# Kernel tuning notes

Hardware: AMD Instinct MI355X
Metric: run time of the kernel (lower is better)

## Reference

```python
import jax, jax.numpy as jnp
import numpy as np

H = 8          # num_heads
BM = 128       # block_size_m
BN = 128       # block_size_n
EPS = 1e-6
CAUSAL = True  # config.causal


def setup_inputs() -> dict:
    key = jax.random.key(0)
    ks = jax.random.split(key, 5)
    B, N, D = 1, 2048, 512
    s = 1.0 / np.sqrt(D)
    # small-scale x so projected points mostly stay inside the Poincare ball
    x = jax.random.normal(ks[0], (B, N, D), jnp.float32) * 0.05
    return {
        'x': x,
        'c': jnp.ones((1,), jnp.float32),
        'Wq': jax.random.normal(ks[1], (D, D), jnp.float32) * s,
        'bq': jnp.zeros((D,), jnp.float32),
        'Wk': jax.random.normal(ks[2], (D, D), jnp.float32) * s,
        'bk': jnp.zeros((D,), jnp.float32),
        'Wv': jax.random.normal(ks[3], (D, D), jnp.float32) * s,
        'bv': jnp.zeros((D,), jnp.float32),
        'Wo': jax.random.normal(ks[4], (D, D), jnp.float32) * s,
        'bo': jnp.zeros((D,), jnp.float32),
    }


def reference(x, c, Wq, bq, Wk, bk, Wv, bv, Wo, bo):
    B, N, D = x.shape
    Dh = D // H
    cc = jnp.clip(jnp.abs(c), 1e-6)            # (1,) learned curvature, abs+clamp as in torch
    sqrt_c = jnp.sqrt(jnp.clip(cc, EPS))

    def proj(W, b):
        return (x @ W + b).reshape(B, N, H, Dh).transpose(0, 2, 1, 3)  # (B,H,N,Dh)

    q, k, v = proj(Wq, bq), proj(Wk, bk), proj(Wv, bv)

    # Poincare distance: ||q-k||^2 expanded via norms (same math as explicit diff tensor)
    qn = (q ** 2).sum(-1)                      # (B,H,N)
    kn = (k ** 2).sum(-1)                      # (B,H,N)
    qk = jnp.einsum('bhmd,bhnd->bhmn', q, k)   # (B,H,N,N)
    diff_sq = jnp.clip(qn[..., :, None] + kn[..., None, :] - 2.0 * qk, 0.0)
    denom = jnp.clip((1.0 - cc * qn)[..., :, None] * (1.0 - cc * kn)[..., None, :], EPS)
    arg = jnp.clip(1.0 + 2.0 * cc * diff_sq / denom, 1.0 + EPS)
    scores = -jnp.arccosh(arg) / sqrt_c        # (B,H,N,N)

    # block-wise softmax: each 128x128 block subtracts ITS OWN max (faithful to torch code,
    # which omits cross-block max rescaling), then exp-sums are accumulated across blocks.
    nbm, nbn = N // BM, N // BN
    s = scores.reshape(B, H, nbm, BM, nbn, BN)
    row = jnp.arange(nbm)[:, None]
    col = jnp.arange(nbn)[None, :]
    skip = (col > row) if CAUSAL else jnp.zeros((nbm, nbn), bool)   # skipped upper blocks
    diag = (col == row) if CAUSAL else jnp.zeros((nbm, nbn), bool)
    tri = jnp.triu(jnp.ones((BM, BN), bool), 1)
    mask = skip[:, None, :, None] | (diag[:, None, :, None] & tri[None, :, None, :])  # (nbm,BM,nbn,BN)

    s_masked = jnp.where(mask, -jnp.inf, s)
    bmax = s_masked.max(axis=-1, keepdims=True)                      # per-block-row max over BN
    bmax = jnp.where(jnp.isfinite(bmax), bmax, 0.0)                  # skipped blocks -> safe
    e = jnp.where(mask, 0.0, jnp.exp(s - bmax))                      # (B,H,nbm,BM,nbn,BN)

    normalizer = jnp.clip(e.sum(axis=(4, 5)).reshape(B, H, N), EPS)  # (B,H,N)
    vb = v.reshape(B, H, nbn, BN, Dh)
    out = jnp.einsum('bhrmcn,bhcnd->bhrmd', e, vb).reshape(B, H, N, Dh)
    out = out / normalizer[..., None]
    out = out.transpose(0, 2, 1, 3).reshape(B, N, D)
    return out @ Wo + bo
```

## Files before the change

### kernel.cpp

```cpp
#include <hip/hip_runtime.h>
#include <math.h>

#define D_MODEL 512
#define NHEADS  8
#define NSEQ    2048
#define NBLK    16
#define NCHUNK  72
#define EPSF    1e-6f
#define WPLANE  262144

typedef _Float16 v8h __attribute__((ext_vector_type(8)));
typedef _Float16 v4h __attribute__((ext_vector_type(4)));
typedef float    v4f __attribute__((ext_vector_type(4)));

static __device__ __forceinline__ v4f mfma16h(v8h a, v8h b, v4f c) {
  return __builtin_amdgcn_mfma_f32_16x16x32_f16(a, b, c, 0, 0, 0);
}

__global__ __launch_bounds__(256) void prep_w(const float* __restrict__ W0,
                                              const float* __restrict__ W1,
                                              const float* __restrict__ W2,
                                              const float* __restrict__ W3,
                                              _Float16* __restrict__ Wth) {
  __shared__ float T[64][68];
  const int z = blockIdx.z;
  const float* W = (z == 0) ? W0 : (z == 1) ? W1 : (z == 2) ? W2 : W3;
  const int kb = blockIdx.x * 64;
  const int nb = blockIdx.y * 64;
  const int tid = threadIdx.x;
#pragma unroll
  for (int l = 0; l < 4; ++l) {
    int f = tid + l * 256;
    int row = f >> 4, c4 = f & 15;
    float4 v = *reinterpret_cast<const float4*>(&W[(size_t)(kb + row) * D_MODEL + nb + c4 * 4]);
    T[c4 * 4 + 0][row] = v.x; T[c4 * 4 + 1][row] = v.y;
    T[c4 * 4 + 2][row] = v.z; T[c4 * 4 + 3][row] = v.w;
  }
  __syncthreads();
  _Float16* oh = Wth + (size_t)z * WPLANE;
#pragma unroll
  for (int l = 0; l < 4; ++l) {
    int f = tid + l * 256;
    int n_ = f >> 4, k4 = f & 15;
    v4h h4;
    h4[0] = (_Float16)T[n_][k4 * 4 + 0];
    h4[1] = (_Float16)T[n_][k4 * 4 + 1];
    h4[2] = (_Float16)T[n_][k4 * 4 + 2];
    h4[3] = (_Float16)T[n_][k4 * 4 + 3];
    *reinterpret_cast<v4h*>(&oh[(size_t)(nb + n_) * D_MODEL + kb + k4 * 4]) = h4;
  }
}

__global__ __launch_bounds__(256) void qkv_gemm(
    const float* __restrict__ x, const _Float16* __restrict__ Wth,
    const float* __restrict__ bq, const float* __restrict__ bk,
    const float* __restrict__ bv,
    _Float16* __restrict__ Qp, _Float16* __restrict__ Kp,
    _Float16* __restrict__ Vp,
    float* __restrict__ Qn_, float* __restrict__ Kn_) {
  __shared__ _Float16 Ah[128][40], Bh[128][40];
  const int z = blockIdx.z;
  const _Float16* Bt = Wth + (size_t)z * WPLANE;
  const float* bias = (z == 0) ? bq : (z == 1) ? bk : bv;
  _Float16* outp = (z == 0) ? Qp : (z == 1) ? Kp : Vp;

  const int bx = blockIdx.x, by = blockIdx.y;
  const int tid = threadIdx.x;
  const int wid = tid >> 6, lane = tid & 63;
  const int wr = wid >> 1, wc = wid & 1;
  const int g = lane >> 4, lx = lane & 15;

  v4f acc[4][4];
#pragma unroll
  for (int i = 0; i < 4; ++i)
#pragma unroll
    for (int j = 0; j < 4; ++j) acc[i][j] = v4f{0.f, 0.f, 0.f, 0.f};

  for (int k0 = 0; k0 < 16; ++k0) {
    __syncthreads();
#pragma unroll
    for (int l = 0; l < 4; ++l) {
      int f = tid + l * 256;
      int row = f >> 3, c4 = f & 7;
      float4 a = *reinterpret_cast<const float4*>(&x[(size_t)(by * 128 + row) * D_MODEL + k0 * 32 + c4 * 4]);
      Ah[row][c4 * 4 + 0] = (_Float16)a.x;
      Ah[row][c4 * 4 + 1] = (_Float16)a.y;
      Ah[row][c4 * 4 + 2] = (_Float16)a.z;
      Ah[row][c4 * 4 + 3] = (_Float16)a.w;
    }
#pragma unroll
    for (int l = 0; l < 2; ++l) {
      int f = tid + l * 256;
      int row = f >> 2, c8 = f & 3;
      *reinterpret_cast<uint4*>(&Bh[row][c8 * 8]) =
          *reinterpret_cast<const uint4*>(&Bt[(size_t)(bx * 128 + row) * D_MODEL + k0 * 32 + c8 * 8]);
    }
    __syncthreads();
    v8h ah[4], bh[4];
#pragma unroll
    for (int i = 0; i < 4; ++i) {
      ah[i] = *reinterpret_cast<const v8h*>(&Ah[wr * 64 + i * 16 + lx][g * 8]);
      bh[i] = *reinterpret_cast<const v8h*>(&Bh[wc * 64 + i * 16 + lx][g * 8]);
    }
#pragma unroll
    for (int i = 0; i < 4; ++i)
#pragma unroll
      for (int j = 0; j < 4; ++j)
        acc[i][j] = mfma16h(ah[i], bh[j], acc[i][j]);
  }

  float np[4][4];
#pragma unroll
  for (int i = 0; i < 4; ++i)
#pragma unroll
    for (int r = 0; r < 4; ++r) np[i][r] = 0.f;

#pragma unroll
  for (int j = 0; j < 4; ++j) {
    const int col = bx * 128 + wc * 64 + j * 16 + lx;
    const float bj = bias[col];
#pragma unroll
    for (int i = 0; i < 4; ++i)
#pragma unroll
      for (int r = 0; r < 4; ++r) {
        const int row = by * 128 + wr * 64 + i * 16 + g * 4 + r;
        float v = acc[i][j][r] + bj;
        _Float16 hv = (_Float16)v;
        outp[(size_t)row * D_MODEL + col] = hv;
        float vr = (float)hv;
        np[i][r] = fmaf(vr, vr, np[i][r]);
      }
  }
  if (z < 2) {
    float* Nout = (z == 0) ? Qn_ : Kn_;
    const int hh = bx * 2 + wc;
#pragma unroll
    for (int i = 0; i < 4; ++i)
#pragma unroll
      for (int r = 0; r < 4; ++r) {
        float s = np[i][r];
        s += __shfl_xor(s, 1, 64);
        s += __shfl_xor(s, 2, 64);
        s += __shfl_xor(s, 4, 64);
        s += __shfl_xor(s, 8, 64);
        if (lx == 0)
          Nout[hh * NSEQ + by * 128 + wr * 64 + i * 16 + g * 4 + r] = s;
      }
  }
}

__global__ __launch_bounds__(256) void vt_prep(const ushort* __restrict__ Vb,
                                               ushort* __restrict__ Vtb) {
  __shared__ ushort T[64][72];
  const int nb = blockIdx.x * 64;
  const int h  = blockIdx.y;
  const int tid = threadIdx.x;
#pragma unroll
  for (int l = 0; l < 2; ++l) {
    int f = tid + l * 256;
    int row = f >> 3, c8 = f & 7;
    uint4 w = *reinterpret_cast<const uint4*>(&Vb[(size_t)(nb + row) * D_MODEL + h * 64 + c8 * 8]);
    const ushort* p = reinterpret_cast<const ushort*>(&w);
#pragma unroll
    for (int j = 0; j < 8; ++j) T[c8 * 8 + j][row] = p[j];
  }
  __syncthreads();
#pragma unroll
  for (int l = 0; l < 2; ++l) {
    int f = tid + l * 256;
    int d = f >> 3, n8 = f & 7;
    *reinterpret_cast<uint4*>(&Vtb[(size_t)(h * 64 + d) * NSEQ + nb + n8 * 8]) =
        *reinterpret_cast<const uint4*>(&T[d][n8 * 8]);
  }
}

__global__ __launch_bounds__(512, 4) void attn(
    const _Float16* __restrict__ Qp, const _Float16* __restrict__ Kp,
    const _Float16* __restrict__ Vtb, const float* __restrict__ Qn,
    const float* __restrict__ Kn, const float* __restrict__ cptr,
    float* __restrict__ Opart, float* __restrict__ Npart)
{
  __shared__ _Float16 Khs[128][68];
  __shared__ _Float16 Vs[64][136];
  __shared__ _Float16 Es[128][136];
  __shared__ float kns[128];

  const int bid = blockIdx.x;
  const int h    = bid & 7;
  const int pid2 = bid >> 3;
  int m = 0, base = 0;
  while (base + (m / 2 + 1) <= pid2) { base += m / 2 + 1; ++m; }
  const int c  = pid2 - base;
  const int n0 = 2 * c;
  const int n1 = (n0 + 1 < m) ? n0 + 1 : m;

  const int tid  = threadIdx.x;
  const int w    = tid >> 6;
  const int lane = tid & 63;
  const int g = lane >> 4, lx = lane & 15;

  const float cc = fmaxf(fabsf(cptr[0]), 1e-6f);
  const float is = rsqrtf(cc);
  const bool is_one = (cc == 1.0f);
  const float two_cc = 2.f * cc;

  const int krow = tid >> 3, kc8 = tid & 7;
  const int vrow = tid >> 4, vc8 = tid & 15;

  const _Float16* Kgh = Kp + h * 64;
  const _Float16* Vgh = Vtb + (size_t)(h * 64) * NSEQ;

  uint4 kpre0, kpre1, vpre0, vpre1;
  float knp = 0.f;
  {
    const _Float16* Kg = Kgh + (size_t)(n0 * 128) * D_MODEL;
    kpre0 = *reinterpret_cast<const uint4*>(&Kg[(size_t)krow * D_MODEL + kc8 * 8]);
    kpre1 = *reinterpret_cast<const uint4*>(&Kg[(size_t)(krow + 64) * D_MODEL + kc8 * 8]);
    vpre0 = *reinterpret_cast<const uint4*>(&Vgh[(size_t)vrow * NSEQ + n0 * 128 + vc8 * 8]);
    vpre1 = *reinterpret_cast<const uint4*>(&Vgh[(size_t)(vrow + 32) * NSEQ + n0 * 128 + vc8 * 8]);
    if (tid < 128) knp = Kn[h * NSEQ + n0 * 128 + tid];
  }
  *reinterpret_cast<uint4*>(&Khs[krow][kc8 * 8]) = kpre0;
  *reinterpret_cast<uint4*>(&Khs[krow + 64][kc8 * 8]) = kpre1;
  *reinterpret_cast<uint4*>(&Vs[vrow][vc8 * 8]) = vpre0;
  *reinterpret_cast<uint4*>(&Vs[vrow + 32][vc8 * 8]) = vpre1;
  if (tid < 128) kns[tid] = knp;
  __syncthreads();

  v8h aQ[2];
  {
    const size_t qoff = (size_t)(m * 128 + 16 * w + lx) * D_MODEL + h * 64 + g * 8;
    aQ[0] = *reinterpret_cast<const v8h*>(&Qp[qoff]);
    aQ[1] = *reinterpret_cast<const v8h*>(&Qp[qoff + 32]);
  }
  float qnr[4], qar[4];
#pragma unroll
  for (int r = 0; r < 4; ++r) {
    qnr[r] = Qn[h * NSEQ + m * 128 + 16 * w + g * 4 + r];
    qar[r] = fmaf(-cc, qnr[r], 1.f);
  }

  v4f o_acc[4];
#pragma unroll
  for (int td = 0; td < 4; ++td) o_acc[td] = v4f{0.f, 0.f, 0.f, 0.f};
  float nrm[4] = {0.f, 0.f, 0.f, 0.f};

  for (int n = n0; n <= n1; ++n) {
    const bool more = (n < n1);
    if (more) {
      const _Float16* Kg = Kgh + (size_t)((n + 1) * 128) * D_MODEL;
      kpre0 = *reinterpret_cast<const uint4*>(&Kg[(size_t)krow * D_MODEL + kc8 * 8]);
      kpre1 = *reinterpret_cast<const uint4*>(&Kg[(size_t)(krow + 64) * D_MODEL + kc8 * 8]);
      vpre0 = *reinterpret_cast<const uint4*>(&Vgh[(size_t)vrow * NSEQ + (n + 1) * 128 + vc8 * 8]);
      vpre1 = *reinterpret_cast<const uint4*>(&Vgh[(size_t)(vrow + 32) * NSEQ + (n + 1) * 128 + vc8 * 8]);
      if (tid < 128) knp = Kn[h * NSEQ + (n + 1) * 128 + tid];
    }

    v4f acc[8];
#pragma unroll
    for (int tn = 0; tn < 8; ++tn) {
      v8h b0 = *reinterpret_cast<const v8h*>(&Khs[tn * 16 + lx][g * 8]);
      v8h b1 = *reinterpret_cast<const v8h*>(&Khs[tn * 16 + lx][g * 8 + 32]);
      v4f a = v4f{0.f, 0.f, 0.f, 0.f};
      a = mfma16h(aQ[0], b0, a);
      a = mfma16h(aQ[1], b1, a);
      acc[tn] = a;
    }

    const bool diag = (n == m);
#pragma unroll
    for (int tn = 0; tn < 8; ++tn) {
      const int col = tn * 16 + lx;
      const float knc = kns[col];
      const float kac = fmaf(-cc, knc, 1.f);
#pragma unroll
      for (int r = 0; r < 4; ++r) {
        const int rowl = 16 * w + g * 4 + r;
        float dsq = fmaxf(fmaf(-2.f, acc[tn][r], qnr[r] + knc), 0.f);
        float den = fmaxf(qar[r] * kac, EPSF);
        float t = fmaxf(two_cc * dsq * __builtin_amdgcn_rcpf(den), EPSF);
        float u = 1.f + t + __builtin_amdgcn_sqrtf(t * (t + 2.f));
        if (diag && col > rowl) u = __builtin_inff();
        acc[tn][r] = u;
      }
    }

    if (is_one) {
      float umin[4] = {__builtin_inff(), __builtin_inff(), __builtin_inff(), __builtin_inff()};
#pragma unroll
      for (int tn = 0; tn < 8; ++tn)
#pragma unroll
        for (int r = 0; r < 4; ++r) umin[r] = fminf(umin[r], acc[tn][r]);
#pragma unroll
      for (int d = 1; d < 16; d <<= 1)
#pragma unroll
        for (int r = 0; r < 4; ++r) umin[r] = fminf(umin[r], __shfl_xor(umin[r], d, 64));
#pragma unroll
      for (int tn = 0; tn < 8; ++tn)
#pragma unroll
        for (int r = 0; r < 4; ++r) {
          float e = umin[r] * __builtin_amdgcn_rcpf(acc[tn][r]);
          nrm[r] += e;
          Es[16 * w + g * 4 + r][tn * 16 + lx] = (_Float16)e;
        }
    } else {
      float smax[4] = {-__builtin_inff(), -__builtin_inff(), -__builtin_inff(), -__builtin_inff()};
#pragma unroll
      for (int tn = 0; tn < 8; ++tn)
#pragma unroll
        for (int r = 0; r < 4; ++r) {
          float s = -__logf(acc[tn][r]) * is;
          acc[tn][r] = s;
          smax[r] = fmaxf(smax[r], s);
        }
#pragma unroll
      for (int d = 1; d < 16; d <<= 1)
#pragma unroll
        for (int r = 0; r < 4; ++r) smax[r] = fmaxf(smax[r], __shfl_xor(smax[r], d, 64));
#pragma unroll
      for (int tn = 0; tn < 8; ++tn)
#pragma unroll
        for (int r = 0; r < 4; ++r) {
          float e = __expf(acc[tn][r] - smax[r]);
          nrm[r] += e;
          Es[16 * w + g * 4 + r][tn * 16 + lx] = (_Float16)e;
        }
    }
    asm volatile("s_waitcnt lgkmcnt(0)" ::: "memory");
    __builtin_amdgcn_sched_barrier(0);

#pragma unroll
    for (int ks = 0; ks < 4; ++ks) {
      v8h ea = *reinterpret_cast<const v8h*>(&Es[16 * w + lx][ks * 32 + g * 8]);
#pragma unroll
      for (int td = 0; td < 4; ++td) {
        v8h vb = *reinterpret_cast<const v8h*>(&Vs[td * 16 + lx][ks * 32 + g * 8]);
        o_acc[td] = mfma16h(ea, vb, o_acc[td]);
      }
    }

    if (more) {
      __syncthreads();
      *reinterpret_cast<uint4*>(&Khs[krow][kc8 * 8]) = kpre0;
      *reinterpret_cast<uint4*>(&Khs[krow + 64][kc8 * 8]) = kpre1;
      *reinterpret_cast<uint4*>(&Vs[vrow][vc8 * 8]) = vpre0;
      *reinterpret_cast<uint4*>(&Vs[vrow + 32][vc8 * 8]) = vpre1;
      if (tid < 128) kns[tid] = knp;
      __syncthreads();
    }
  }

#pragma unroll
  for (int d = 1; d < 16; d <<= 1)
#pragma unroll
    for (int r = 0; r < 4; ++r) nrm[r] += __shfl_xor(nrm[r], d, 64);

  float* Op = Opart + ((size_t)h * NCHUNK + pid2) * (128 * 64);
#pragma unroll
  for (int td = 0; td < 4; ++td)
#pragma unroll
    for (int r = 0; r < 4; ++r)
      Op[(size_t)(16 * w + g * 4 + r) * 64 + td * 16 + lx] = o_acc[td][r];
  if (lx == 0) {
#pragma unroll
    for (int r = 0; r < 4; ++r)
      Npart[((size_t)h * NCHUNK + pid2) * 128 + 16 * w + g * 4 + r] = nrm[r];
  }
}

__global__ __launch_bounds__(256) void reduce_o(const float* __restrict__ Opart,
                                                const float* __restrict__ Npart,
                                                _Float16* __restrict__ Of) {
  const int mq = blockIdx.x;
  const int mm = mq >> 2;
  const int rq = (mq & 3) * 32;
  const int h  = blockIdx.y;
  const int tid = threadIdx.x;
  int base = 0;
  for (int k = 0; k < mm; ++k) base += k / 2 + 1;
  const int nch = mm / 2 + 1;

  __shared__ float innorm[32];
  if (tid < 32) {
    float s = 0.f;
    for (int cI = 0; cI < nch; ++cI)
      s += Npart[((size_t)h * NCHUNK + base + cI) * 128 + rq + tid];
    innorm[tid] = 1.f / fmaxf(s, EPSF);
  }
  __syncthreads();
#pragma unroll
  for (int l = 0; l < 2; ++l) {
    int f = tid + l * 256;
    int r = f >> 4, c4 = f & 15;
    float4 s = {0.f, 0.f, 0.f, 0.f};
    for (int cI = 0; cI < nch; ++cI) {
      const float4 p = *reinterpret_cast<const float4*>(
          &Opart[((size_t)h * NCHUNK + base + cI) * 8192 + (size_t)(rq + r) * 64 + c4 * 4]);
      s.x += p.x; s.y += p.y; s.z += p.z; s.w += p.w;
    }
    float inv = innorm[r];
    v4h o4;
    o4[0] = (_Float16)(s.x * inv); o4[1] = (_Float16)(s.y * inv);
    o4[2] = (_Float16)(s.z * inv); o4[3] = (_Float16)(s.w * inv);
    *reinterpret_cast<v4h*>(
        &Of[(size_t)(mm * 128 + rq + r) * D_MODEL + h * 64 + c4 * 4]) = o4;
  }
}

__global__ __launch_bounds__(256) void o_gemm(const _Float16* __restrict__ Of,
                                              const _Float16* __restrict__ Wth,
                                              const float* __restrict__ bo,
                                              float* __restrict__ out) {
  __shared__ _Float16 As[64][40], Bs[64][40];
  const _Float16* Bt = Wth + (size_t)3 * WPLANE;
  const int bx = blockIdx.x, by = blockIdx.y;
  const int tid = threadIdx.x;
  const int wid = tid >> 6, lane = tid & 63;
  const int wr = wid >> 1, wc = wid & 1;
  const int g = lane >> 4, lx = lane & 15;

  v4f acc[2][2];
#pragma unroll
  for (int i = 0; i < 2; ++i)
#pragma unroll
    for (int j = 0; j < 2; ++j) acc[i][j] = v4f{0.f, 0.f, 0.f, 0.f};

  const int srow = tid >> 2, sc8 = tid & 3;
  for (int k0 = 0; k0 < 16; ++k0) {
    __syncthreads();
    *reinterpret_cast<uint4*>(&As[srow][sc8 * 8]) =
        *reinterpret_cast<const uint4*>(&Of[(size_t)(by * 64 + srow) * D_MODEL + k0 * 32 + sc8 * 8]);
    *reinterpret_cast<uint4*>(&Bs[srow][sc8 * 8]) =
        *reinterpret_cast<const uint4*>(&Bt[(size_t)(bx * 64 + srow) * D_MODEL + k0 * 32 + sc8 * 8]);
    __syncthreads();
    v8h ah[2][2], bh[2][2];
#pragma unroll
    for (int i = 0; i < 2; ++i) {
      ah[i][0] = *reinterpret_cast<const v8h*>(&As[wr * 32 + i * 16 + lx][g * 8]);
      bh[i][0] = *reinterpret_cast<const v8h*>(&Bs[wc * 32 + i * 16 + lx][g * 8]);
    }
#pragma unroll
    for (int i = 0; i < 2; ++i)
#pragma unroll
      for (int j = 0; j < 2; ++j)
        acc[i][j] = mfma16h(ah[i][0], bh[j][0], acc[i][j]);
  }
#pragma unroll
  for (int j = 0; j < 2; ++j) {
    const int col = bx * 64 + wc * 32 + j * 16 + lx;
    const float bj = bo[col];
#pragma unroll
    for (int i = 0; i < 2; ++i)
#pragma unroll
      for (int r = 0; r < 4; ++r) {
        const int row = by * 64 + wr * 32 + i * 16 + g * 4 + r;
        out[(size_t)row * D_MODEL + col] = acc[i][j][r] + bj;
      }
  }
}

extern "C" void kernel_launch(void* const* d_in, const int* in_sizes, int n_in,
                              void* d_out, int out_size, void* d_ws, size_t ws_size,
                              hipStream_t stream) {
  (void)in_sizes; (void)n_in; (void)out_size; (void)ws_size;
  const float* x  = (const float*)d_in[0];
  const float* cfg= (const float*)d_in[1];
  const float* Wq = (const float*)d_in[2];
  const float* bq = (const float*)d_in[3];
  const float* Wk = (const float*)d_in[4];
  const float* bk = (const float*)d_in[5];
  const float* Wv = (const float*)d_in[6];
  const float* bv = (const float*)d_in[7];
  const float* Wo = (const float*)d_in[8];
  const float* bo = (const float*)d_in[9];
  float* out = (float*)d_out;

  char* p = (char*)d_ws;
  const size_t PL = (size_t)NSEQ * D_MODEL * sizeof(_Float16);
  _Float16* Wth = (_Float16*)p;        p += 4 * (size_t)WPLANE * sizeof(_Float16);
  _Float16* Qp  = (_Float16*)p;        p += PL;
  _Float16* Kp  = (_Float16*)p;        p += PL;
  _Float16* Vp  = (_Float16*)p;        p += PL;
  _Float16* Vtb = (_Float16*)p;        p += PL;
  _Float16* Of  = (_Float16*)p;        p += PL;
  float*  Qn  = (float*)p;             p += (size_t)NHEADS * NSEQ * sizeof(float);
  float*  Kn  = (float*)p;             p += (size_t)NHEADS * NSEQ * sizeof(float);
  float*  Opart = (float*)p;           p += (size_t)NHEADS * NCHUNK * 8192 * sizeof(float);
  float*  Npart = (float*)p;

  prep_w<<<dim3(8, 8, 4), 256, 0, stream>>>(Wq, Wk, Wv, Wo, Wth);
  qkv_gemm<<<dim3(4, 16, 3), 256, 0, stream>>>(x, Wth, bq, bk, bv,
                                               Qp, Kp, Vp, Qn, Kn);
  vt_prep<<<dim3(32, 8), 256, 0, stream>>>((const ushort*)Vp, (ushort*)Vtb);
  attn<<<dim3(NCHUNK * NHEADS), 512, 0, stream>>>(Qp, Kp, Vtb, Qn, Kn, cfg,
                                                  Opart, Npart);
  reduce_o<<<dim3(64, NHEADS), 256, 0, stream>>>(Opart, Npart, Of);
  o_gemm<<<dim3(8, 32), 256, 0, stream>>>(Of, Wth, bo, out);
}
```

Measured before the change: 86.67 us.

## Fuse V transpose into QKV GEMM, shrink attention LDS, store fp16 partials

The V projection is now written transposed straight from the QKV GEMM epilogue, which removes the separate vt_prep kernel and its launch. The attention kernel splits the E tile into per-wave halves so it uses less LDS, raises the occupancy hint to 6, and adds s_setprio around the MFMA sections. Partial outputs are stored as fp16 instead of fp32, halving the write and read traffic between attn and reduce_o. The transposed V stores are uncoalesced, and fp16 partials lose some precision.

```diff
diff --git a/kernel.cpp b/kernel.cpp
--- a/kernel.cpp
+++ b/kernel.cpp
@@ -56,13 +56,13 @@
     const float* __restrict__ bq, const float* __restrict__ bk,
     const float* __restrict__ bv,
     _Float16* __restrict__ Qp, _Float16* __restrict__ Kp,
-    _Float16* __restrict__ Vp,
+    _Float16* __restrict__ Vtb,
     float* __restrict__ Qn_, float* __restrict__ Kn_) {
   __shared__ _Float16 Ah[128][40], Bh[128][40];
   const int z = blockIdx.z;
   const _Float16* Bt = Wth + (size_t)z * WPLANE;
   const float* bias = (z == 0) ? bq : (z == 1) ? bk : bv;
-  _Float16* outp = (z == 0) ? Qp : (z == 1) ? Kp : Vp;
+  _Float16* outp = (z == 0) ? Qp : Kp;
 
   const int bx = blockIdx.x, by = blockIdx.y;
   const int tid = threadIdx.x;
@@ -126,7 +126,8 @@
         const int row = by * 128 + wr * 64 + i * 16 + g * 4 + r;
         float v = acc[i][j][r] + bj;
         _Float16 hv = (_Float16)v;
-        outp[(size_t)row * D_MODEL + col] = hv;
+        if (z == 2) Vtb[(size_t)col * NSEQ + row] = hv;
+        else        outp[(size_t)row * D_MODEL + col] = hv;
         float vr = (float)hv;
         np[i][r] = fmaf(vr, vr, np[i][r]);
       }
@@ -149,40 +150,15 @@
   }
 }
 
-__global__ __launch_bounds__(256) void vt_prep(const ushort* __restrict__ Vb,
-                                               ushort* __restrict__ Vtb) {
-  __shared__ ushort T[64][72];
-  const int nb = blockIdx.x * 64;
-  const int h  = blockIdx.y;
-  const int tid = threadIdx.x;
-#pragma unroll
-  for (int l = 0; l < 2; ++l) {
-    int f = tid + l * 256;
-    int row = f >> 3, c8 = f & 7;
-    uint4 w = *reinterpret_cast<const uint4*>(&Vb[(size_t)(nb + row) * D_MODEL + h * 64 + c8 * 8]);
-    const ushort* p = reinterpret_cast<const ushort*>(&w);
-#pragma unroll
-    for (int j = 0; j < 8; ++j) T[c8 * 8 + j][row] = p[j];
-  }
-  __syncthreads();
-#pragma unroll
-  for (int l = 0; l < 2; ++l) {
-    int f = tid + l * 256;
-    int d = f >> 3, n8 = f & 7;
-    *reinterpret_cast<uint4*>(&Vtb[(size_t)(h * 64 + d) * NSEQ + nb + n8 * 8]) =
-        *reinterpret_cast<const uint4*>(&T[d][n8 * 8]);
-  }
-}
-
-__global__ __launch_bounds__(512, 4) void attn(
+__global__ __launch_bounds__(512, 6) void attn(
     const _Float16* __restrict__ Qp, const _Float16* __restrict__ Kp,
     const _Float16* __restrict__ Vtb, const float* __restrict__ Qn,
     const float* __restrict__ Kn, const float* __restrict__ cptr,
-    float* __restrict__ Opart, float* __restrict__ Npart)
+    _Float16* __restrict__ Opart, float* __restrict__ Npart)
 {
   __shared__ _Float16 Khs[128][68];
-  __shared__ _Float16 Vs[64][136];
-  __shared__ _Float16 Es[128][136];
+  __shared__ _Float16 Vs[64][140];
+  __shared__ _Float16 Es[8][16][68];
   __shared__ float kns[128];
 
   const int bid = blockIdx.x;
@@ -257,6 +233,7 @@
     }
 
     v4f acc[8];
+    __builtin_amdgcn_s_setprio(1);
 #pragma unroll
     for (int tn = 0; tn < 8; ++tn) {
       v8h b0 = *reinterpret_cast<const v8h*>(&Khs[tn * 16 + lx][g * 8]);
@@ -266,6 +243,7 @@
       a = mfma16h(aQ[1], b1, a);
       acc[tn] = a;
     }
+    __builtin_amdgcn_s_setprio(0);
 
     const bool diag = (n == m);
 #pragma unroll
@@ -285,58 +263,62 @@
       }
     }
 
+    float mred[4];
     if (is_one) {
-      float umin[4] = {__builtin_inff(), __builtin_inff(), __builtin_inff(), __builtin_inff()};
+#pragma unroll
+      for (int r = 0; r < 4; ++r) mred[r] = __builtin_inff();
 #pragma unroll
       for (int tn = 0; tn < 8; ++tn)
 #pragma unroll
-        for (int r = 0; r < 4; ++r) umin[r] = fminf(umin[r], acc[tn][r]);
+        for (int r = 0; r < 4; ++r) mred[r] = fminf(mred[r], acc[tn][r]);
 #pragma unroll
       for (int d = 1; d < 16; d <<= 1)
 #pragma unroll
-        for (int r = 0; r < 4; ++r) umin[r] = fminf(umin[r], __shfl_xor(umin[r], d, 64));
-#pragma unroll
-      for (int tn = 0; tn < 8; ++tn)
-#pragma unroll
-        for (int r = 0; r < 4; ++r) {
-          float e = umin[r] * __builtin_amdgcn_rcpf(acc[tn][r]);
-          nrm[r] += e;
-          Es[16 * w + g * 4 + r][tn * 16 + lx] = (_Float16)e;
-        }
+        for (int r = 0; r < 4; ++r) mred[r] = fminf(mred[r], __shfl_xor(mred[r], d, 64));
     } else {
-      float smax[4] = {-__builtin_inff(), -__builtin_inff(), -__builtin_inff(), -__builtin_inff()};
+#pragma unroll
+      for (int r = 0; r < 4; ++r) mred[r] = -__builtin_inff();
 #pragma unroll
       for (int tn = 0; tn < 8; ++tn)
 #pragma unroll
         for (int r = 0; r < 4; ++r) {
           float s = -__logf(acc[tn][r]) * is;
           acc[tn][r] = s;
-          smax[r] = fmaxf(smax[r], s);
+          mred[r] = fmaxf(mred[r], s);
         }
 #pragma unroll
       for (int d = 1; d < 16; d <<= 1)
 #pragma unroll
-        for (int r = 0; r < 4; ++r) smax[r] = fmaxf(smax[r], __shfl_xor(smax[r], d, 64));
-#pragma unroll
-      for (int tn = 0; tn < 8; ++tn)
+        for (int r = 0; r < 4; ++r) mred[r] = fmaxf(mred[r], __shfl_xor(mred[r], d, 64));
+    }
+
+#pragma unroll
+    for (int half = 0; half < 2; ++half) {
+#pragma unroll
+      for (int tn2 = 0; tn2 < 4; ++tn2) {
+        const int tn = half * 4 + tn2;
 #pragma unroll
         for (int r = 0; r < 4; ++r) {
-          float e = __expf(acc[tn][r] - smax[r]);
+          float e = is_one ? mred[r] * __builtin_amdgcn_rcpf(acc[tn][r])
+                           : __expf(acc[tn][r] - mred[r]);
           nrm[r] += e;
-          Es[16 * w + g * 4 + r][tn * 16 + lx] = (_Float16)e;
+          Es[w][g * 4 + r][tn2 * 16 + lx] = (_Float16)e;
         }
-    }
-    asm volatile("s_waitcnt lgkmcnt(0)" ::: "memory");
-    __builtin_amdgcn_sched_barrier(0);
-
-#pragma unroll
-    for (int ks = 0; ks < 4; ++ks) {
-      v8h ea = *reinterpret_cast<const v8h*>(&Es[16 * w + lx][ks * 32 + g * 8]);
-#pragma unroll
-      for (int td = 0; td < 4; ++td) {
-        v8h vb = *reinterpret_cast<const v8h*>(&Vs[td * 16 + lx][ks * 32 + g * 8]);
-        o_acc[td] = mfma16h(ea, vb, o_acc[td]);
-      }
+      }
+      asm volatile("s_waitcnt lgkmcnt(0)" ::: "memory");
+      __builtin_amdgcn_sched_barrier(0);
+      __builtin_amdgcn_s_setprio(1);
+#pragma unroll
+      for (int ks2 = 0; ks2 < 2; ++ks2) {
+        const int ks = half * 2 + ks2;
+        v8h ea = *reinterpret_cast<const v8h*>(&Es[w][lx][ks2 * 32 + g * 8]);
+#pragma unroll
+        for (int td = 0; td < 4; ++td) {
+          v8h vb = *reinterpret_cast<const v8h*>(&Vs[td * 16 + lx][ks * 32 + g * 8]);
+          o_acc[td] = mfma16h(ea, vb, o_acc[td]);
+        }
+      }
+      __builtin_amdgcn_s_setprio(0);
     }
 
     if (more) {
@@ -355,12 +337,12 @@
 #pragma unroll
     for (int r = 0; r < 4; ++r) nrm[r] += __shfl_xor(nrm[r], d, 64);
 
-  float* Op = Opart + ((size_t)h * NCHUNK + pid2) * (128 * 64);
+  _Float16* Op = Opart + ((size_t)h * NCHUNK + pid2) * (128 * 64);
 #pragma unroll
   for (int td = 0; td < 4; ++td)
 #pragma unroll
     for (int r = 0; r < 4; ++r)
-      Op[(size_t)(16 * w + g * 4 + r) * 64 + td * 16 + lx] = o_acc[td][r];
+      Op[(size_t)(16 * w + g * 4 + r) * 64 + td * 16 + lx] = (_Float16)o_acc[td][r];
   if (lx == 0) {
 #pragma unroll
     for (int r = 0; r < 4; ++r)
@@ -368,7 +350,7 @@
   }
 }
 
-__global__ __launch_bounds__(256) void reduce_o(const float* __restrict__ Opart,
+__global__ __launch_bounds__(256) void reduce_o(const _Float16* __restrict__ Opart,
                                                 const float* __restrict__ Npart,
                                                 _Float16* __restrict__ Of) {
   const int mq = blockIdx.x;
@@ -392,16 +374,16 @@
   for (int l = 0; l < 2; ++l) {
     int f = tid + l * 256;
     int r = f >> 4, c4 = f & 15;
-    float4 s = {0.f, 0.f, 0.f, 0.f};
+    float s0 = 0.f, s1 = 0.f, s2 = 0.f, s3 = 0.f;
     for (int cI = 0; cI < nch; ++cI) {
-      const float4 p = *reinterpret_cast<const float4*>(
+      const v4h p = *reinterpret_cast<const v4h*>(
           &Opart[((size_t)h * NCHUNK + base + cI) * 8192 + (size_t)(rq + r) * 64 + c4 * 4]);
-      s.x += p.x; s.y += p.y; s.z += p.z; s.w += p.w;
+      s0 += (float)p[0]; s1 += (float)p[1]; s2 += (float)p[2]; s3 += (float)p[3];
     }
     float inv = innorm[r];
     v4h o4;
-    o4[0] = (_Float16)(s.x * inv); o4[1] = (_Float16)(s.y * inv);
-    o4[2] = (_Float16)(s.z * inv); o4[3] = (_Float16)(s.w * inv);
+    o4[0] = (_Float16)(s0 * inv); o4[1] = (_Float16)(s1 * inv);
+    o4[2] = (_Float16)(s2 * inv); o4[3] = (_Float16)(s3 * inv);
     *reinterpret_cast<v4h*>(
         &Of[(size_t)(mm * 128 + rq + r) * D_MODEL + h * 64 + c4 * 4]) = o4;
   }
@@ -433,17 +415,17 @@
     *reinterpret_cast<uint4*>(&Bs[srow][sc8 * 8]) =
         *reinterpret_cast<const uint4*>(&Bt[(size_t)(bx * 64 + srow) * D_MODEL + k0 * 32 + sc8 * 8]);
     __syncthreads();
-    v8h ah[2][2], bh[2][2];
+    v8h ah[2], bh[2];
 #pragma unroll
     for (int i = 0; i < 2; ++i) {
-      ah[i][0] = *reinterpret_cast<const v8h*>(&As[wr * 32 + i * 16 + lx][g * 8]);
-      bh[i][0] = *reinterpret_cast<const v8h*>(&Bs[wc * 32 + i * 16 + lx][g * 8]);
+      ah[i] = *reinterpret_cast<const v8h*>(&As[wr * 32 + i * 16 + lx][g * 8]);
+      bh[i] = *reinterpret_cast<const v8h*>(&Bs[wc * 32 + i * 16 + lx][g * 8]);
     }
 #pragma unroll
     for (int i = 0; i < 2; ++i)
 #pragma unroll
       for (int j = 0; j < 2; ++j)
-        acc[i][j] = mfma16h(ah[i][0], bh[j][0], acc[i][j]);
+        acc[i][j] = mfma16h(ah[i], bh[j], acc[i][j]);
   }
 #pragma unroll
   for (int j = 0; j < 2; ++j) {
@@ -480,18 +462,16 @@
   _Float16* Wth = (_Float16*)p;        p += 4 * (size_t)WPLANE * sizeof(_Float16);
   _Float16* Qp  = (_Float16*)p;        p += PL;
   _Float16* Kp  = (_Float16*)p;        p += PL;
-  _Float16* Vp  = (_Float16*)p;        p += PL;
   _Float16* Vtb = (_Float16*)p;        p += PL;
   _Float16* Of  = (_Float16*)p;        p += PL;
   float*  Qn  = (float*)p;             p += (size_t)NHEADS * NSEQ * sizeof(float);
   float*  Kn  = (float*)p;             p += (size_t)NHEADS * NSEQ * sizeof(float);
-  float*  Opart = (float*)p;           p += (size_t)NHEADS * NCHUNK * 8192 * sizeof(float);
+  _Float16* Opart = (_Float16*)p;      p += (size_t)NHEADS * NCHUNK * 8192 * sizeof(_Float16);
   float*  Npart = (float*)p;
 
   prep_w<<<dim3(8, 8, 4), 256, 0, stream>>>(Wq, Wk, Wv, Wo, Wth);
   qkv_gemm<<<dim3(4, 16, 3), 256, 0, stream>>>(x, Wth, bq, bk, bv,
-                                               Qp, Kp, Vp, Qn, Kn);
-  vt_prep<<<dim3(32, 8), 256, 0, stream>>>((const ushort*)Vp, (ushort*)Vtb);
+                                               Qp, Kp, Vtb, Qn, Kn);
   attn<<<dim3(NCHUNK * NHEADS), 512, 0, stream>>>(Qp, Kp, Vtb, Qn, Kn, cfg,
                                                   Opart, Npart);
   reduce_o<<<dim3(64, NHEADS), 256, 0, stream>>>(Opart, Npart, Of);
```

New measurement: 104.5 us. +20.6%, slower.
